# Kernel optimization log

Measured on AMD Instinct MI355X. Metric: run time of the kernel, lower is better.

The kernel has to match this reference:

```python
import jax, jax.numpy as jnp
import numpy as np

N = 100_000      # nodes
E = 1_600_000    # directed edges (before self-loops)
F_IN = 128       # input node features
H = 4            # attention heads
C = 64           # hidden channels (concat=False -> heads averaged)
NEG_SLOPE = 0.2
BN_EPS = 1e-5


def setup_inputs() -> dict:
    key = jax.random.key(0)
    ks = jax.random.split(key, 16)
    s = 0.05
    return {
        "x": jax.random.normal(ks[0], (N, F_IN), dtype=jnp.float32),
        "edge_index": jax.random.randint(ks[1], (2, E), 0, N, dtype=jnp.int64),
        # GAT layer params: layer 0 has F_IN inputs, layers 1..2 have C inputs
        "W0": jax.random.normal(ks[2], (F_IN, H * C), dtype=jnp.float32) * s,
        "Wl": jax.random.normal(ks[3], (2, C, H * C), dtype=jnp.float32) * s,
        "att_src": jax.random.normal(ks[4], (3, H, C), dtype=jnp.float32) * s,
        "att_dst": jax.random.normal(ks[5], (3, H, C), dtype=jnp.float32) * s,
        "conv_bias": jnp.zeros((3, C), dtype=jnp.float32),
        # BatchNorm1d (inference: running stats)
        "bn_gamma": jnp.ones((3, C), dtype=jnp.float32),
        "bn_beta": jnp.zeros((3, C), dtype=jnp.float32),
        "bn_mean": jax.random.normal(ks[6], (3, C), dtype=jnp.float32) * 0.1,
        "bn_var": jax.random.uniform(ks[7], (3, C), dtype=jnp.float32, minval=0.5, maxval=1.5),
        # MLP head
        "lin1_w": jax.random.normal(ks[8], (C, C // 2), dtype=jnp.float32) * s,
        "lin1_b": jnp.zeros((C // 2,), dtype=jnp.float32),
        "lin2_w": jax.random.normal(ks[9], (C // 2, 1), dtype=jnp.float32) * s,
        "lin2_b": jnp.zeros((1,), dtype=jnp.float32),
    }


def _gat_layer(x, src, dst, W, a_src, a_dst, bias):
    # x: [N, Fin] -> h: [N, H, C]
    h = (x @ W).reshape(-1, H, C)
    # per-node attention logits, gathered per edge: [Etot, H]
    e_src = jnp.einsum("nhc,hc->nh", h, a_src)
    e_dst = jnp.einsum("nhc,hc->nh", h, a_dst)
    e = jax.nn.leaky_relu(e_src[src] + e_dst[dst], NEG_SLOPE)
    # softmax over incoming edges of each target node (self-loops guarantee non-empty)
    e_max = jax.ops.segment_max(e, dst, num_segments=N)
    w = jnp.exp(e - e_max[dst])                              # [Etot, H]
    denom = jax.ops.segment_sum(w, dst, num_segments=N)      # [N, H]
    # weighted scatter-add of gathered source features
    msg = h[src] * w[:, :, None]                             # [Etot, H, C]
    out = jax.ops.segment_sum(msg, dst, num_segments=N)      # [N, H, C]
    out = out / denom[:, :, None]
    return out.mean(axis=1) + bias                           # concat=False -> head mean


def reference(x, edge_index, W0, Wl, att_src, att_dst, conv_bias,
              bn_gamma, bn_beta, bn_mean, bn_var,
              lin1_w, lin1_b, lin2_w, lin2_b):
    # add self-loops (PyG GATConv default)
    loop = jnp.arange(N, dtype=edge_index.dtype)
    src = jnp.concatenate([edge_index[0], loop])
    dst = jnp.concatenate([edge_index[1], loop])

    Ws = [W0, Wl[0], Wl[1]]
    for l in range(3):
        x = _gat_layer(x, src, dst, Ws[l], att_src[l], att_dst[l], conv_bias[l])
        x = (x - bn_mean[l]) * (bn_gamma[l] / jnp.sqrt(bn_var[l] + BN_EPS)) + bn_beta[l]
        x = jax.nn.relu(x)  # dropout is identity in inference

    x = jax.nn.relu(x @ lin1_w + lin1_b)
    x = x @ lin2_w + lin2_b
    return x.squeeze(-1)
```

## Files before the change

### kernel.cpp

```cpp
#include <hip/hip_runtime.h>
#include <hip/hip_bf16.h>
#include <cstdint>

#define N_NODES 100000
#define N_EDGES 1600000
#define N_TOT   1700000
#define HEADS   4
#define CH      64
#define HC      256
#define NEG     0.2f
#define BNEPS   1e-5f
#define NPART   8
#define PART_N  12500
#define CHUNK_E 16384

typedef __attribute__((ext_vector_type(8))) short short8;
typedef __attribute__((ext_vector_type(4))) float f32x4;

static __device__ __forceinline__ float lrelu(float x) {
    return x > 0.f ? x : NEG * x;
}
static __device__ __forceinline__ unsigned short f2bf(float f) {
    unsigned int u = __float_as_uint(f);
    unsigned int r = (u + 0x7fffu + ((u >> 16) & 1u)) >> 16;
    return (unsigned short)r;
}
static __device__ __forceinline__ float bflo(unsigned int v) { return __uint_as_float(v << 16); }
static __device__ __forceinline__ float bfhi(unsigned int v) { return __uint_as_float(v & 0xffff0000u); }

__global__ void detect_dtype(const int* ei32, int* flag) {
    int l = threadIdx.x;
    int v = ei32[2 * l + 1];
    unsigned long long b = __ballot(v == 0);
    if (l == 0) *flag = (__popcll(b) >= 48) ? 1 : 0;
}

static __device__ __forceinline__ int edge_at(const void* ei, int is64, long long pos) {
    if (is64) return (int)((const long long*)ei)[pos];
    return ((const int*)ei)[pos];
}

__global__ void convert_k(const void* ei, const int* flag, int* src32, int* dst32) {
    int e = blockIdx.x * 256 + threadIdx.x;
    if (e >= N_TOT) return;
    int is64 = *flag;
    if (e < N_EDGES) {
        src32[e] = edge_at(ei, is64, e);
        dst32[e] = edge_at(ei, is64, (long long)N_EDGES + e);
    } else {
        int v = e - N_EDGES;
        src32[e] = v; dst32[e] = v;
    }
}

__global__ void hist_part_k(const int* __restrict__ dst32, int* __restrict__ counts) {
    int part = blockIdx.x & (NPART - 1), chunk = blockIdx.x / NPART;
    int lo = part * PART_N, hi = lo + PART_N;
    int base = chunk * CHUNK_E;
    int end = min(base + CHUNK_E, N_TOT);
    for (int i = base + threadIdx.x; i < end; i += 256) {
        int d = dst32[i];
        if (d >= lo && d < hi) atomicAdd(&counts[d], 1);
    }
}

__global__ void scan_block(const int* in, int* out, int* bsum) {
    __shared__ int sm[256];
    int t = threadIdx.x;
    int i = blockIdx.x * 256 + t;
    int v = (i < N_NODES) ? in[i] : 0;
    int acc = v;
    sm[t] = v; __syncthreads();
    for (int d = 1; d < 256; d <<= 1) {
        int add = (t >= d) ? sm[t - d] : 0;
        __syncthreads();
        acc += add; sm[t] = acc;
        __syncthreads();
    }
    if (i < N_NODES) out[i] = acc - v;
    if (t == 255) bsum[blockIdx.x] = acc;
}

__global__ void scan_bsum(int* bsum, int nb) {
    __shared__ int sm[512];
    int t = threadIdx.x;
    int v = (t < nb) ? bsum[t] : 0;
    int acc = v;
    sm[t] = v; __syncthreads();
    for (int d = 1; d < 512; d <<= 1) {
        int add = (t >= d) ? sm[t - d] : 0;
        __syncthreads();
        acc += add; sm[t] = acc;
        __syncthreads();
    }
    if (t < nb) bsum[t] = acc - v;
}

__global__ void scan_add(int* off, const int* bsum, int* fill) {
    int i = blockIdx.x * 256 + threadIdx.x;
    if (i < N_NODES) {
        int v = off[i] + bsum[blockIdx.x];
        off[i] = v; fill[i] = v;
    }
    if (i == 0) off[N_NODES] = N_TOT;
}

__global__ void scatter_part_k(const int* __restrict__ src32, const int* __restrict__ dst32,
                               int* __restrict__ fill, int* __restrict__ csr) {
    int part = blockIdx.x & (NPART - 1), chunk = blockIdx.x / NPART;
    int lo = part * PART_N, hi = lo + PART_N;
    int base = chunk * CHUNK_E;
    int end = min(base + CHUNK_E, N_TOT);
    for (int i = base + threadIdx.x; i < end; i += 256) {
        int d = dst32[i];
        if (d >= lo && d < hi) {
            int s = src32[i];
            int pos = atomicAdd(&fill[d], 1);
            csr[pos] = s;
        }
    }
}

__global__ void wconv_k(const float* __restrict__ w, unsigned short* __restrict__ wb, int n) {
    int i = blockIdx.x * 256 + threadIdx.x;
    if (i < n) wb[i] = f2bf(w[i]);
}

template<int K>
__global__ __launch_bounds__(256) void gemm_mfma_k(const float* __restrict__ A,
                                                   const unsigned short* __restrict__ Wb,
                                                   const float* __restrict__ as,
                                                   const float* __restrict__ ad,
                                                   unsigned short* __restrict__ hb,
                                                   float* __restrict__ es,
                                                   float* __restrict__ ed) {
    __shared__ unsigned short Bs[256 * K];
    __shared__ unsigned short As[64 * K];
    int t = threadIdx.x;
    int bm = blockIdx.x * 64;

    for (int idx4 = t; idx4 < K * 64; idx4 += 256) {
        int k = idx4 >> 6;
        int c = (idx4 & 63) * 4;
        ushort4 wv = *(const ushort4*)(Wb + (size_t)k * HC + c);
        Bs[((c + 0) * K + k) ^ ((((c + 0) & 7)) << 3)] = wv.x;
        Bs[((c + 1) * K + k) ^ ((((c + 1) & 7)) << 3)] = wv.y;
        Bs[((c + 2) * K + k) ^ ((((c + 2) & 7)) << 3)] = wv.z;
        Bs[((c + 3) * K + k) ^ ((((c + 3) & 7)) << 3)] = wv.w;
    }
    {
        int row = t >> 2, seg = t & 3;
        int grow = bm + row;
        const float* Ar = A + (size_t)grow * K + seg * (K / 4);
        #pragma unroll
        for (int f = 0; f < K / 16; ++f) {
            float4 v = make_float4(0.f, 0.f, 0.f, 0.f);
            if (grow < N_NODES) v = *(const float4*)(Ar + f * 4);
            ushort4 b;
            b.x = f2bf(v.x); b.y = f2bf(v.y); b.z = f2bf(v.z); b.w = f2bf(v.w);
            int idx = (row * K + seg * (K / 4) + f * 4) ^ ((row & 7) << 3);
            *(ushort4*)(&As[idx]) = b;
        }
    }
    __syncthreads();

    int w = t >> 6, lane = t & 63;
    int c16 = lane & 15, kg = lane >> 4;
    int swz = (c16 & 7) << 3;
    f32x4 acc[4][4];
    #pragma unroll
    for (int i = 0; i < 4; ++i)
        #pragma unroll
        for (int j = 0; j < 4; ++j) acc[i][j] = (f32x4)(0.f);

    #pragma unroll
    for (int kc = 0; kc < K / 32; ++kc) {
        int ko = kc * 32 + kg * 8;
        short8 af[4], bf[4];
        #pragma unroll
        for (int rs = 0; rs < 4; ++rs)
            af[rs] = *(const short8*)(&As[((16 * rs + c16) * K + ko) ^ swz]);
        #pragma unroll
        for (int ct = 0; ct < 4; ++ct) {
            int col = w * 64 + ct * 16 + c16;
            bf[ct] = *(const short8*)(&Bs[(col * K + ko) ^ swz]);
        }
        #pragma unroll
        for (int rs = 0; rs < 4; ++rs)
            #pragma unroll
            for (int ct = 0; ct < 4; ++ct)
                acc[rs][ct] = __builtin_amdgcn_mfma_f32_16x16x32_bf16(af[rs], bf[ct], acc[rs][ct], 0, 0, 0);
    }

    float asv[4], adv[4];
    #pragma unroll
    for (int ct = 0; ct < 4; ++ct) {
        asv[ct] = as[w * 64 + ct * 16 + c16];
        adv[ct] = ad[w * 64 + ct * 16 + c16];
    }
    #pragma unroll
    for (int rs = 0; rs < 4; ++rs) {
        float esr[4], edr[4];
        #pragma unroll
        for (int reg = 0; reg < 4; ++reg) {
            float s = 0.f, d = 0.f;
            #pragma unroll
            for (int ct = 0; ct < 4; ++ct) {
                s += acc[rs][ct][reg] * asv[ct];
                d += acc[rs][ct][reg] * adv[ct];
            }
            #pragma unroll
            for (int sh = 1; sh < 16; sh <<= 1) {
                s += __shfl_xor(s, sh);
                d += __shfl_xor(d, sh);
            }
            esr[reg] = s; edr[reg] = d;
        }
        int r0 = bm + rs * 16 + kg * 4;
        if (c16 == 0) {
            #pragma unroll
            for (int reg = 0; reg < 4; ++reg) {
                if (r0 + reg < N_NODES) {
                    es[(size_t)(r0 + reg) * 4 + w] = esr[reg];
                    ed[(size_t)(r0 + reg) * 4 + w] = edr[reg];
                }
            }
        }
        #pragma unroll
        for (int ct = 0; ct < 4; ++ct)
            #pragma unroll
            for (int reg = 0; reg < 4; ++reg) {
                int grow = r0 + reg;
                if (grow < N_NODES)
                    hb[(size_t)grow * HC + w * 64 + ct * 16 + c16] = f2bf(acc[rs][ct][reg]);
            }
    }
}

__global__ __launch_bounds__(256) void aggregate_k(const unsigned short* __restrict__ h,
                                                   const float* __restrict__ es,
                                                   const float* __restrict__ ed,
                                                   const int* __restrict__ off,
                                                   const int* __restrict__ csr,
                                                   const float* __restrict__ bias,
                                                   const float* __restrict__ g,
                                                   const float* __restrict__ bb,
                                                   const float* __restrict__ mu,
                                                   const float* __restrict__ var,
                                                   float* __restrict__ xout) {
    __shared__ float wbuf[4][64][4];
    __shared__ int   sbuf[4][64];
    int wv = threadIdx.x >> 6;
    int lane = threadIdx.x & 63;
    int wid = blockIdx.x * 4 + wv;
    if (wid >= N_NODES) return;

    int s0 = off[wid], s1 = off[wid + 1];
    float4 edv = *(const float4*)(ed + (size_t)wid * 4);

    int q = lane >> 4;
    int s16 = lane & 15;
    int head = s16 >> 2;
    float ds0 = 0.f, ds1 = 0.f, ds2 = 0.f, ds3 = 0.f;
    float a[16];
    #pragma unroll
    for (int i = 0; i < 16; ++i) a[i] = 0.f;

    for (int base = s0; base < s1; base += 64) {
        int e = base + lane;
        float w0 = 0.f, w1 = 0.f, w2 = 0.f, w3 = 0.f;
        int s = 0;
        if (e < s1) {
            s = csr[e];
            float4 ev = *(const float4*)(es + (size_t)s * 4);
            w0 = __expf(fminf(lrelu(ev.x + edv.x), 80.f));
            w1 = __expf(fminf(lrelu(ev.y + edv.y), 80.f));
            w2 = __expf(fminf(lrelu(ev.z + edv.z), 80.f));
            w3 = __expf(fminf(lrelu(ev.w + edv.w), 80.f));
        }
        ds0 += w0; ds1 += w1; ds2 += w2; ds3 += w3;
        *(float4*)(&wbuf[wv][lane][0]) = make_float4(w0, w1, w2, w3);
        sbuf[wv][lane] = s;
        asm volatile("" ::: "memory");

        int cnt = min(64, s1 - base);
        for (int j = 0; j < cnt; j += 4) {
            int jj = j + q;
            if (jj < cnt) {
                int   ss = sbuf[wv][jj];
                float wm = wbuf[wv][jj][head];
                const unsigned short* hp = h + (size_t)ss * HC + s16 * 16;
                uint4 h0 = *(const uint4*)hp;
                uint4 h1 = *(const uint4*)(hp + 8);
                a[0]  = fmaf(wm, bflo(h0.x), a[0]);  a[1]  = fmaf(wm, bfhi(h0.x), a[1]);
                a[2]  = fmaf(wm, bflo(h0.y), a[2]);  a[3]  = fmaf(wm, bfhi(h0.y), a[3]);
                a[4]  = fmaf(wm, bflo(h0.z), a[4]);  a[5]  = fmaf(wm, bfhi(h0.z), a[5]);
                a[6]  = fmaf(wm, bflo(h0.w), a[6]);  a[7]  = fmaf(wm, bfhi(h0.w), a[7]);
                a[8]  = fmaf(wm, bflo(h1.x), a[8]);  a[9]  = fmaf(wm, bfhi(h1.x), a[9]);
                a[10] = fmaf(wm, bflo(h1.y), a[10]); a[11] = fmaf(wm, bfhi(h1.y), a[11]);
                a[12] = fmaf(wm, bflo(h1.z), a[12]); a[13] = fmaf(wm, bfhi(h1.z), a[13]);
                a[14] = fmaf(wm, bflo(h1.w), a[14]); a[15] = fmaf(wm, bfhi(h1.w), a[15]);
            }
        }
        asm volatile("" ::: "memory");
    }

    #pragma unroll
    for (int i = 0; i < 16; ++i) {
        a[i] += __shfl_xor(a[i], 16);
        a[i] += __shfl_xor(a[i], 32);
    }
    #pragma unroll
    for (int d = 1; d < 64; d <<= 1) {
        ds0 += __shfl_xor(ds0, d); ds1 += __shfl_xor(ds1, d);
        ds2 += __shfl_xor(ds2, d); ds3 += __shfl_xor(ds3, d);
    }
    float den = head == 0 ? ds0 : head == 1 ? ds1 : head == 2 ? ds2 : ds3;
    float inv = 1.f / den;
    #pragma unroll
    for (int i = 0; i < 16; ++i) a[i] *= inv;
    #pragma unroll
    for (int i = 0; i < 16; ++i) {
        a[i] += __shfl_xor(a[i], 4);
        a[i] += __shfl_xor(a[i], 8);
    }

    if (lane < 4) {
        int c0 = lane * 16;
        float o[16];
        #pragma unroll
        for (int v4 = 0; v4 < 4; ++v4) {
            int c = c0 + v4 * 4;
            float4 bi = *(const float4*)(bias + c);
            float4 gv = *(const float4*)(g + c);
            float4 bv = *(const float4*)(bb + c);
            float4 mv = *(const float4*)(mu + c);
            float4 vv = *(const float4*)(var + c);
            o[v4 * 4 + 0] = fmaxf((a[v4 * 4 + 0] * 0.25f + bi.x - mv.x) * (gv.x * rsqrtf(vv.x + BNEPS)) + bv.x, 0.f);
            o[v4 * 4 + 1] = fmaxf((a[v4 * 4 + 1] * 0.25f + bi.y - mv.y) * (gv.y * rsqrtf(vv.y + BNEPS)) + bv.y, 0.f);
            o[v4 * 4 + 2] = fmaxf((a[v4 * 4 + 2] * 0.25f + bi.z - mv.z) * (gv.z * rsqrtf(vv.z + BNEPS)) + bv.z, 0.f);
            o[v4 * 4 + 3] = fmaxf((a[v4 * 4 + 3] * 0.25f + bi.w - mv.w) * (gv.w * rsqrtf(vv.w + BNEPS)) + bv.w, 0.f);
        }
        #pragma unroll
        for (int v4 = 0; v4 < 4; ++v4)
            *(float4*)(xout + (size_t)wid * CH + c0 + v4 * 4) =
                make_float4(o[v4 * 4 + 0], o[v4 * 4 + 1], o[v4 * 4 + 2], o[v4 * 4 + 3]);
    }
}

__global__ __launch_bounds__(256) void mlp_k(const float* __restrict__ x,
                                             const float* __restrict__ w1,
                                             const float* __restrict__ b1,
                                             const float* __restrict__ w2,
                                             const float* __restrict__ b2,
                                             float* __restrict__ out) {
    __shared__ float w1s[CH * 32];
    __shared__ float w2s[32];
    __shared__ float b1s[32];
    int t = threadIdx.x;
    for (int i = t; i < CH * 32; i += 256) w1s[i] = w1[i];
    if (t < 32) { w2s[t] = w2[t]; b1s[t] = b1[t]; }
    __syncthreads();
    int n = blockIdx.x * 256 + t;
    if (n >= N_NODES) return;
    float y[32];
    #pragma unroll
    for (int j = 0; j < 32; ++j) y[j] = b1s[j];
    const float* xr = x + (size_t)n * CH;
    for (int c4 = 0; c4 < 16; ++c4) {
        float4 xv = *(const float4*)(xr + c4 * 4);
        const float* wr = &w1s[c4 * 4 * 32];
        #pragma unroll
        for (int j = 0; j < 32; ++j)
            y[j] += xv.x * wr[j] + xv.y * wr[32 + j] + xv.z * wr[64 + j] + xv.w * wr[96 + j];
    }
    float o = b2[0];
    #pragma unroll
    for (int j = 0; j < 32; ++j) o += fmaxf(y[j], 0.f) * w2s[j];
    out[n] = o;
}

extern "C" void kernel_launch(void* const* d_in, const int* in_sizes, int n_in,
                              void* d_out, int out_size, void* d_ws, size_t ws_size,
                              hipStream_t stream) {
    const float* x0    = (const float*)d_in[0];
    const void*  ei    = d_in[1];
    const float* W0    = (const float*)d_in[2];
    const float* Wl    = (const float*)d_in[3];
    const float* asrc  = (const float*)d_in[4];
    const float* adst  = (const float*)d_in[5];
    const float* cbias = (const float*)d_in[6];
    const float* bng   = (const float*)d_in[7];
    const float* bnb   = (const float*)d_in[8];
    const float* bnm   = (const float*)d_in[9];
    const float* bnv   = (const float*)d_in[10];
    const float* l1w   = (const float*)d_in[11];
    const float* l1b   = (const float*)d_in[12];
    const float* l2w   = (const float*)d_in[13];
    const float* l2b   = (const float*)d_in[14];
    float* out = (float*)d_out;

    char* p = (char*)d_ws;
    auto alloc = [&](size_t bytes) { char* r = p; p += (bytes + 255) & ~(size_t)255; return r; };
    unsigned short* hb  = (unsigned short*)alloc((size_t)N_NODES * HC * 2);
    unsigned short* wbf = (unsigned short*)alloc((size_t)128 * HC * 2);
    float* xA   = (float*)alloc((size_t)N_NODES * CH * 4);
    float* xB   = (float*)alloc((size_t)N_NODES * CH * 4);
    float* es   = (float*)alloc((size_t)N_NODES * 4 * 4);
    float* ed   = (float*)alloc((size_t)N_NODES * 4 * 4);
    int* counts = (int*)alloc((size_t)N_NODES * 4);
    int* off    = (int*)alloc((size_t)(N_NODES + 1) * 4);
    int* fill   = (int*)alloc((size_t)N_NODES * 4);
    int* bsum   = (int*)alloc(512 * 4);
    int* flag   = (int*)alloc(256);
    int* src32  = (int*)alloc((size_t)N_TOT * 4);
    int* dst32  = (int*)alloc((size_t)N_TOT * 4);
    int* csr    = (int*)alloc((size_t)N_TOT * 4);

    int nbScan = (N_NODES + 255) / 256;
    int nchunk = (N_TOT + CHUNK_E - 1) / CHUNK_E;
    hipMemsetAsync(counts, 0, (size_t)N_NODES * 4, stream);
    detect_dtype<<<1, 64, 0, stream>>>((const int*)ei, flag);
    convert_k<<<(N_TOT + 255) / 256, 256, 0, stream>>>(ei, flag, src32, dst32);
    hist_part_k<<<nchunk * NPART, 256, 0, stream>>>(dst32, counts);
    scan_block<<<nbScan, 256, 0, stream>>>(counts, off, bsum);
    scan_bsum<<<1, 512, 0, stream>>>(bsum, nbScan);
    scan_add<<<nbScan, 256, 0, stream>>>(off, bsum, fill);
    scatter_part_k<<<nchunk * NPART, 256, 0, stream>>>(src32, dst32, fill, csr);

    const float* xin = x0;
    const float* W = W0;
    float* xbufs[2] = {xA, xB};
    int ngemm = (N_NODES + 63) / 64;
    for (int l = 0; l < 3; ++l) {
        int K = (l == 0) ? 128 : 64;
        wconv_k<<<(K * HC + 255) / 256, 256, 0, stream>>>(W, wbf, K * HC);
        if (l == 0)
            gemm_mfma_k<128><<<ngemm, 256, 0, stream>>>(xin, wbf, asrc + l * HC, adst + l * HC, hb, es, ed);
        else
            gemm_mfma_k<64><<<ngemm, 256, 0, stream>>>(xin, wbf, asrc + l * HC, adst + l * HC, hb, es, ed);
        float* xo = xbufs[l & 1];
        aggregate_k<<<(N_NODES + 3) / 4, 256, 0, stream>>>(hb, es, ed, off, csr,
            cbias + l * CH, bng + l * CH, bnb + l * CH, bnm + l * CH, bnv + l * CH, xo);
        xin = xo;
        W = Wl + (size_t)l * CH * HC;
    }
    mlp_k<<<(N_NODES + 255) / 256, 256, 0, stream>>>(xin, l1w, l1b, l2w, l2b, out);
}
```

Before: 773.7 us.

## Fuse edge conversion with histogram, fold weight cast into GEMM, restructure aggregation

After: 747.4 us. 3.4% less time.

```diff
diff --git a/kernel.cpp b/kernel.cpp
--- a/kernel.cpp
+++ b/kernel.cpp
@@ -40,28 +40,17 @@
     return ((const int*)ei)[pos];
 }
 
-__global__ void convert_k(const void* ei, const int* flag, int* src32, int* dst32) {
+__global__ void convert_hist_k(const void* ei, const int* flag,
+                               int* __restrict__ src32, int* __restrict__ dst32,
+                               int* __restrict__ counts) {
     int e = blockIdx.x * 256 + threadIdx.x;
     if (e >= N_TOT) return;
     int is64 = *flag;
-    if (e < N_EDGES) {
-        src32[e] = edge_at(ei, is64, e);
-        dst32[e] = edge_at(ei, is64, (long long)N_EDGES + e);
-    } else {
-        int v = e - N_EDGES;
-        src32[e] = v; dst32[e] = v;
-    }
-}
-
-__global__ void hist_part_k(const int* __restrict__ dst32, int* __restrict__ counts) {
-    int part = blockIdx.x & (NPART - 1), chunk = blockIdx.x / NPART;
-    int lo = part * PART_N, hi = lo + PART_N;
-    int base = chunk * CHUNK_E;
-    int end = min(base + CHUNK_E, N_TOT);
-    for (int i = base + threadIdx.x; i < end; i += 256) {
-        int d = dst32[i];
-        if (d >= lo && d < hi) atomicAdd(&counts[d], 1);
-    }
+    int s, d;
+    if (e < N_EDGES) { s = edge_at(ei, is64, e); d = edge_at(ei, is64, (long long)N_EDGES + e); }
+    else { int v = e - N_EDGES; s = v; d = v; }
+    src32[e] = s; dst32[e] = d;
+    atomicAdd(&counts[d], 1);
 }
 
 __global__ void scan_block(const int* in, int* out, int* bsum) {
@@ -121,14 +110,9 @@
     }
 }
 
-__global__ void wconv_k(const float* __restrict__ w, unsigned short* __restrict__ wb, int n) {
-    int i = blockIdx.x * 256 + threadIdx.x;
-    if (i < n) wb[i] = f2bf(w[i]);
-}
-
 template<int K>
 __global__ __launch_bounds__(256) void gemm_mfma_k(const float* __restrict__ A,
-                                                   const unsigned short* __restrict__ Wb,
+                                                   const float* __restrict__ Wf,
                                                    const float* __restrict__ as,
                                                    const float* __restrict__ ad,
                                                    unsigned short* __restrict__ hb,
@@ -142,11 +126,11 @@
     for (int idx4 = t; idx4 < K * 64; idx4 += 256) {
         int k = idx4 >> 6;
         int c = (idx4 & 63) * 4;
-        ushort4 wv = *(const ushort4*)(Wb + (size_t)k * HC + c);
-        Bs[((c + 0) * K + k) ^ ((((c + 0) & 7)) << 3)] = wv.x;
-        Bs[((c + 1) * K + k) ^ ((((c + 1) & 7)) << 3)] = wv.y;
-        Bs[((c + 2) * K + k) ^ ((((c + 2) & 7)) << 3)] = wv.z;
-        Bs[((c + 3) * K + k) ^ ((((c + 3) & 7)) << 3)] = wv.w;
+        float4 wv = *(const float4*)(Wf + (size_t)k * HC + c);
+        Bs[((c + 0) * K + k) ^ ((((c + 0) & 7)) << 3)] = f2bf(wv.x);
+        Bs[((c + 1) * K + k) ^ ((((c + 1) & 7)) << 3)] = f2bf(wv.y);
+        Bs[((c + 2) * K + k) ^ ((((c + 2) & 7)) << 3)] = f2bf(wv.z);
+        Bs[((c + 3) * K + k) ^ ((((c + 3) & 7)) << 3)] = f2bf(wv.w);
     }
     {
         int row = t >> 2, seg = t & 3;
@@ -258,13 +242,12 @@
     int s0 = off[wid], s1 = off[wid + 1];
     float4 edv = *(const float4*)(ed + (size_t)wid * 4);
 
-    int q = lane >> 4;
-    int s16 = lane & 15;
-    int head = s16 >> 2;
+    int half = lane >> 5;
+    int sub  = lane & 31;
+    int head = sub >> 3;
     float ds0 = 0.f, ds1 = 0.f, ds2 = 0.f, ds3 = 0.f;
-    float a[16];
-    #pragma unroll
-    for (int i = 0; i < 16; ++i) a[i] = 0.f;
+    float a0 = 0.f, a1 = 0.f, a2 = 0.f, a3 = 0.f, a4 = 0.f, a5 = 0.f, a6 = 0.f, a7 = 0.f;
+    const unsigned short* hsub = h + sub * 8;
 
     for (int base = s0; base < s1; base += 64) {
         int e = base + lane;
@@ -284,32 +267,29 @@
         asm volatile("" ::: "memory");
 
         int cnt = min(64, s1 - base);
-        for (int j = 0; j < cnt; j += 4) {
-            int jj = j + q;
-            if (jj < cnt) {
-                int   ss = sbuf[wv][jj];
-                float wm = wbuf[wv][jj][head];
-                const unsigned short* hp = h + (size_t)ss * HC + s16 * 16;
-                uint4 h0 = *(const uint4*)hp;
-                uint4 h1 = *(const uint4*)(hp + 8);
-                a[0]  = fmaf(wm, bflo(h0.x), a[0]);  a[1]  = fmaf(wm, bfhi(h0.x), a[1]);
-                a[2]  = fmaf(wm, bflo(h0.y), a[2]);  a[3]  = fmaf(wm, bfhi(h0.y), a[3]);
-                a[4]  = fmaf(wm, bflo(h0.z), a[4]);  a[5]  = fmaf(wm, bfhi(h0.z), a[5]);
-                a[6]  = fmaf(wm, bflo(h0.w), a[6]);  a[7]  = fmaf(wm, bfhi(h0.w), a[7]);
-                a[8]  = fmaf(wm, bflo(h1.x), a[8]);  a[9]  = fmaf(wm, bfhi(h1.x), a[9]);
-                a[10] = fmaf(wm, bflo(h1.y), a[10]); a[11] = fmaf(wm, bfhi(h1.y), a[11]);
-                a[12] = fmaf(wm, bflo(h1.z), a[12]); a[13] = fmaf(wm, bfhi(h1.z), a[13]);
-                a[14] = fmaf(wm, bflo(h1.w), a[14]); a[15] = fmaf(wm, bfhi(h1.w), a[15]);
-            }
+        int jj = half;
+        int scur = (jj < cnt) ? sbuf[wv][jj] : sbuf[wv][0];
+        float wcur = (jj < cnt) ? wbuf[wv][jj][head] : 0.f;
+        uint4 hv = *(const uint4*)(hsub + (size_t)scur * HC);
+        for (int j = 0; j < cnt; j += 2) {
+            int jn = j + 2 + half;
+            int snx = (jn < cnt) ? sbuf[wv][jn] : sbuf[wv][0];
+            float wnx = (jn < cnt) ? wbuf[wv][jn][head] : 0.f;
+            uint4 hn = *(const uint4*)(hsub + (size_t)snx * HC);
+            a0 = fmaf(wcur, bflo(hv.x), a0); a1 = fmaf(wcur, bfhi(hv.x), a1);
+            a2 = fmaf(wcur, bflo(hv.y), a2); a3 = fmaf(wcur, bfhi(hv.y), a3);
+            a4 = fmaf(wcur, bflo(hv.z), a4); a5 = fmaf(wcur, bfhi(hv.z), a5);
+            a6 = fmaf(wcur, bflo(hv.w), a6); a7 = fmaf(wcur, bfhi(hv.w), a7);
+            hv = hn; wcur = wnx;
         }
         asm volatile("" ::: "memory");
     }
 
-    #pragma unroll
-    for (int i = 0; i < 16; ++i) {
-        a[i] += __shfl_xor(a[i], 16);
-        a[i] += __shfl_xor(a[i], 32);
-    }
+    a0 += __shfl_xor(a0, 32); a1 += __shfl_xor(a1, 32);
+    a2 += __shfl_xor(a2, 32); a3 += __shfl_xor(a3, 32);
+    a4 += __shfl_xor(a4, 32); a5 += __shfl_xor(a5, 32);
+    a6 += __shfl_xor(a6, 32); a7 += __shfl_xor(a7, 32);
+
     #pragma unroll
     for (int d = 1; d < 64; d <<= 1) {
         ds0 += __shfl_xor(ds0, d); ds1 += __shfl_xor(ds1, d);
@@ -317,34 +297,39 @@
     }
     float den = head == 0 ? ds0 : head == 1 ? ds1 : head == 2 ? ds2 : ds3;
     float inv = 1.f / den;
-    #pragma unroll
-    for (int i = 0; i < 16; ++i) a[i] *= inv;
-    #pragma unroll
-    for (int i = 0; i < 16; ++i) {
-        a[i] += __shfl_xor(a[i], 4);
-        a[i] += __shfl_xor(a[i], 8);
-    }
-
-    if (lane < 4) {
-        int c0 = lane * 16;
-        float o[16];
-        #pragma unroll
-        for (int v4 = 0; v4 < 4; ++v4) {
-            int c = c0 + v4 * 4;
-            float4 bi = *(const float4*)(bias + c);
-            float4 gv = *(const float4*)(g + c);
-            float4 bv = *(const float4*)(bb + c);
-            float4 mv = *(const float4*)(mu + c);
-            float4 vv = *(const float4*)(var + c);
-            o[v4 * 4 + 0] = fmaxf((a[v4 * 4 + 0] * 0.25f + bi.x - mv.x) * (gv.x * rsqrtf(vv.x + BNEPS)) + bv.x, 0.f);
-            o[v4 * 4 + 1] = fmaxf((a[v4 * 4 + 1] * 0.25f + bi.y - mv.y) * (gv.y * rsqrtf(vv.y + BNEPS)) + bv.y, 0.f);
-            o[v4 * 4 + 2] = fmaxf((a[v4 * 4 + 2] * 0.25f + bi.z - mv.z) * (gv.z * rsqrtf(vv.z + BNEPS)) + bv.z, 0.f);
-            o[v4 * 4 + 3] = fmaxf((a[v4 * 4 + 3] * 0.25f + bi.w - mv.w) * (gv.w * rsqrtf(vv.w + BNEPS)) + bv.w, 0.f);
-        }
-        #pragma unroll
-        for (int v4 = 0; v4 < 4; ++v4)
-            *(float4*)(xout + (size_t)wid * CH + c0 + v4 * 4) =
-                make_float4(o[v4 * 4 + 0], o[v4 * 4 + 1], o[v4 * 4 + 2], o[v4 * 4 + 3]);
+    a0 *= inv; a1 *= inv; a2 *= inv; a3 *= inv;
+    a4 *= inv; a5 *= inv; a6 *= inv; a7 *= inv;
+
+    a0 += __shfl_xor(a0, 8);  a1 += __shfl_xor(a1, 8);
+    a2 += __shfl_xor(a2, 8);  a3 += __shfl_xor(a3, 8);
+    a4 += __shfl_xor(a4, 8);  a5 += __shfl_xor(a5, 8);
+    a6 += __shfl_xor(a6, 8);  a7 += __shfl_xor(a7, 8);
+    a0 += __shfl_xor(a0, 16); a1 += __shfl_xor(a1, 16);
+    a2 += __shfl_xor(a2, 16); a3 += __shfl_xor(a3, 16);
+    a4 += __shfl_xor(a4, 16); a5 += __shfl_xor(a5, 16);
+    a6 += __shfl_xor(a6, 16); a7 += __shfl_xor(a7, 16);
+
+    if (lane < 8) {
+        int c = lane * 8;
+        float av[8] = {a0, a1, a2, a3, a4, a5, a6, a7};
+        float4 bi0 = *(const float4*)(bias + c), bi1 = *(const float4*)(bias + c + 4);
+        float4 gv0 = *(const float4*)(g + c),    gv1 = *(const float4*)(g + c + 4);
+        float4 bv0 = *(const float4*)(bb + c),   bv1 = *(const float4*)(bb + c + 4);
+        float4 mv0 = *(const float4*)(mu + c),   mv1 = *(const float4*)(mu + c + 4);
+        float4 vv0 = *(const float4*)(var + c),  vv1 = *(const float4*)(var + c + 4);
+        float bia[8] = {bi0.x, bi0.y, bi0.z, bi0.w, bi1.x, bi1.y, bi1.z, bi1.w};
+        float gg[8]  = {gv0.x, gv0.y, gv0.z, gv0.w, gv1.x, gv1.y, gv1.z, gv1.w};
+        float be[8]  = {bv0.x, bv0.y, bv0.z, bv0.w, bv1.x, bv1.y, bv1.z, bv1.w};
+        float mm[8]  = {mv0.x, mv0.y, mv0.z, mv0.w, mv1.x, mv1.y, mv1.z, mv1.w};
+        float vv[8]  = {vv0.x, vv0.y, vv0.z, vv0.w, vv1.x, vv1.y, vv1.z, vv1.w};
+        float o[8];
+        #pragma unroll
+        for (int k = 0; k < 8; ++k) {
+            float t0 = (av[k] * 0.25f + bia[k] - mm[k]) * (gg[k] * rsqrtf(vv[k] + BNEPS)) + be[k];
+            o[k] = fmaxf(t0, 0.f);
+        }
+        *(float4*)(xout + (size_t)wid * CH + c)     = make_float4(o[0], o[1], o[2], o[3]);
+        *(float4*)(xout + (size_t)wid * CH + c + 4) = make_float4(o[4], o[5], o[6], o[7]);
     }
 }
 
@@ -403,7 +388,6 @@
     char* p = (char*)d_ws;
     auto alloc = [&](size_t bytes) { char* r = p; p += (bytes + 255) & ~(size_t)255; return r; };
     unsigned short* hb  = (unsigned short*)alloc((size_t)N_NODES * HC * 2);
-    unsigned short* wbf = (unsigned short*)alloc((size_t)128 * HC * 2);
     float* xA   = (float*)alloc((size_t)N_NODES * CH * 4);
     float* xB   = (float*)alloc((size_t)N_NODES * CH * 4);
     float* es   = (float*)alloc((size_t)N_NODES * 4 * 4);
@@ -421,8 +405,7 @@
     int nchunk = (N_TOT + CHUNK_E - 1) / CHUNK_E;
     hipMemsetAsync(counts, 0, (size_t)N_NODES * 4, stream);
     detect_dtype<<<1, 64, 0, stream>>>((const int*)ei, flag);
-    convert_k<<<(N_TOT + 255) / 256, 256, 0, stream>>>(ei, flag, src32, dst32);
-    hist_part_k<<<nchunk * NPART, 256, 0, stream>>>(dst32, counts);
+    convert_hist_k<<<(N_TOT + 255) / 256, 256, 0, stream>>>(ei, flag, src32, dst32, counts);
     scan_block<<<nbScan, 256, 0, stream>>>(counts, off, bsum);
     scan_bsum<<<1, 512, 0, stream>>>(bsum, nbScan);
     scan_add<<<nbScan, 256, 0, stream>>>(off, bsum, fill);
@@ -433,12 +416,10 @@
     float* xbufs[2] = {xA, xB};
     int ngemm = (N_NODES + 63) / 64;
     for (int l = 0; l < 3; ++l) {
-        int K = (l == 0) ? 128 : 64;
-        wconv_k<<<(K * HC + 255) / 256, 256, 0, stream>>>(W, wbf, K * HC);
         if (l == 0)
-            gemm_mfma_k<128><<<ngemm, 256, 0, stream>>>(xin, wbf, asrc + l * HC, adst + l * HC, hb, es, ed);
+            gemm_mfma_k<128><<<ngemm, 256, 0, stream>>>(xin, W, asrc + l * HC, adst + l * HC, hb, es, ed);
         else
-            gemm_mfma_k<64><<<ngemm, 256, 0, stream>>>(xin, wbf, asrc + l * HC, adst + l * HC, hb, es, ed);
+            gemm_mfma_k<64><<<ngemm, 256, 0, stream>>>(xin, W, asrc + l * HC, adst + l * HC, hb, es, ed);
         float* xo = xbufs[l & 1];
         aggregate_k<<<(N_NODES + 3) / 4, 256, 0, stream>>>(hb, es, ed, off, csr,
             cbias + l * CH, bng + l * CH, bnb + l * CH, bnm + l * CH, bnv + l * CH, xo);
```
